# Performance work log

Measured on AMD Instinct MI355X. Metric: run time of the kernel, lower is better.

## Reference

```python
import jax, jax.numpy as jnp
import numpy as np

B, N, F, D, K = 128, 512, 64, 64, 20  # batch, nodes, input_dim, dim, topk


def setup_inputs() -> dict:
    key = jax.random.key(0)
    ks = jax.random.split(key, 9)
    s = 1.0 / np.sqrt(D)
    return dict(
        data=jax.random.normal(ks[0], (B, N, F), jnp.float32),
        org_edge_index=jax.random.randint(ks[1], (2, 1024), 0, N),
        embed=jax.random.normal(ks[2], (N, D), jnp.float32),
        W_lin=jax.random.normal(ks[3], (F, D), jnp.float32) / np.sqrt(F),
        att_i=jax.random.normal(ks[4], (D,), jnp.float32) * s,
        att_j=jax.random.normal(ks[5], (D,), jnp.float32) * s,
        att_em_i=jax.random.normal(ks[6], (D,), jnp.float32) * s,
        att_em_j=jax.random.normal(ks[7], (D,), jnp.float32) * s,
        gnn_bias=jnp.zeros((D,), jnp.float32),
        bn1_gamma=jnp.ones((D,), jnp.float32),
        bn1_beta=jnp.zeros((D,), jnp.float32),
        bn2_gamma=jnp.ones((D,), jnp.float32),
        bn2_beta=jnp.zeros((D,), jnp.float32),
        out_W=jax.random.normal(ks[8], (D, 1), jnp.float32) * s,
        out_b=jnp.zeros((1,), jnp.float32),
    )


def reference(data, embed, W_lin, att_i, att_j, att_em_i, att_em_j, gnn_bias,
              bn1_gamma, bn1_beta, bn2_gamma, bn2_beta, out_W, out_b,
              org_edge_index):
    eps = 1e-5
    slope = 0.2  # LeakyReLU negative slope (PyG GATConv default)
    BN_ = B * N

    # Encoder -> learned graph: cosine similarity + topk (GDN-style)
    e_norm = embed / (jnp.linalg.norm(embed, axis=-1, keepdims=True) + 1e-12)
    weight_arr = e_norm @ e_norm.T                      # [N, N]
    _, topk_idx = jax.lax.top_k(weight_arr, K)          # [N, K]

    src = topk_idx.reshape(-1)                          # gated_j (message source)
    dst = jnp.repeat(jnp.arange(N), K)                  # gated_i (message dest)
    self_mask = src == dst                              # remove_self_loops

    # batched edge index (block-diagonal over batch)
    offs = (jnp.arange(B) * N)[:, None]
    src_b = (src[None, :] + offs).reshape(-1)
    dst_b = (dst[None, :] + offs).reshape(-1)
    mask_b = jnp.tile(self_mask, B)

    # add_self_loops for all B*N nodes
    loops = jnp.arange(BN_)
    src_all = jnp.concatenate([src_b, loops])
    dst_all = jnp.concatenate([dst_b, loops])
    mask_all = jnp.concatenate([mask_b, jnp.zeros((BN_,), bool)])

    # GraphLayer: linear transform + embedding-augmented attention
    x = data.reshape(BN_, F)
    g = x @ W_lin                                       # [BN, D]
    emb_all = jnp.tile(embed, (B, 1))                   # [BN, D]
    s_i = g @ att_i + emb_all @ att_em_i                # per-node dest score
    s_j = g @ att_j + emb_all @ att_em_j                # per-node src score
    logits = jax.nn.leaky_relu(s_i[dst_all] + s_j[src_all], slope)
    logits = jnp.where(mask_all, -jnp.inf, logits)      # removed self edges

    # softmax over incoming edges of each destination node
    m = jax.ops.segment_max(logits, dst_all, num_segments=BN_)
    ex = jnp.exp(logits - m[dst_all])
    denom = jax.ops.segment_sum(ex, dst_all, num_segments=BN_)
    attn = ex / denom[dst_all]

    agg = jax.ops.segment_sum(g[src_all] * attn[:, None], dst_all,
                              num_segments=BN_) + gnn_bias  # [BN, D]

    # BatchNorm1d (batch stats) + ReLU
    mu = agg.mean(0)
    var = agg.var(0)
    h = jax.nn.relu((agg - mu) / jnp.sqrt(var + eps) * bn1_gamma + bn1_beta)

    # multiply by node embedding, channel BN over (batch, node), ReLU
    h = h.reshape(B, N, D) * embed[None]
    mu2 = h.mean(axis=(0, 1))
    var2 = h.var(axis=(0, 1))
    h = jax.nn.relu((h - mu2) / jnp.sqrt(var2 + eps) * bn2_gamma + bn2_beta)

    # OutLayer (layer_num=1): Linear(D, 1)
    out = (h @ out_W + out_b).reshape(B, N)
    return out
```

## Files before the change

kernel.cpp:

```cpp
#include <hip/hip_runtime.h>
#include <math.h>

#define Bsz 128
#define Nn  512
#define Fd  64
#define Dd  64
#define Kk  20
#define BN  (Bsz*Nn)
#define NCPY 32
#define ET_STRIDE 129
#define SMEM_BYTES (64*ET_STRIDE*4 + 256*4)

__device__ __forceinline__ float leaky(float v){ return (v >= 0.f) ? v : 0.2f*v; }

__device__ __forceinline__ int wave_argmax_idx(float v, int idx){
  int vi = __float_as_int(v);
#define DPP_STEP(CTRL) { \
    int nv = __builtin_amdgcn_update_dpp(vi,  vi,  CTRL, 0xF, 0xF, false); \
    int ni = __builtin_amdgcn_update_dpp(idx, idx, CTRL, 0xF, 0xF, false); \
    float fnv = __int_as_float(nv), fov = __int_as_float(vi); \
    bool take = (fnv > fov) || ((fnv == fov) && (ni < idx)); \
    vi = take ? nv : vi; idx = take ? ni : idx; \
  }
  DPP_STEP(0x111)
  DPP_STEP(0x112)
  DPP_STEP(0x114)
  DPP_STEP(0x118)
  DPP_STEP(0x142)
  DPP_STEP(0x143)
#undef DPP_STEP
  return __builtin_amdgcn_readlane(idx, 63);
}

__global__ __launch_bounds__(256) void k1(const float* __restrict__ x,
    const float* __restrict__ W, const float* __restrict__ embed,
    const float* __restrict__ att_i, const float* __restrict__ att_j,
    const float* __restrict__ aem_i, const float* __restrict__ aem_j,
    float* __restrict__ g, float* __restrict__ s_i, float* __restrict__ s_j,
    int* __restrict__ topk){
  __shared__ __align__(16) char smem[SMEM_BYTES];
  int tid = threadIdx.x, b = blockIdx.x;

  if (b >= 128){
    int bl = b - 128;
    float4* sW   = (float4*)smem;
    float4* sai  = (float4*)(smem + 16384);
    float4* saj  = sai + 16;
    float4* semi = saj + 16;
    float4* semj = semi + 16;
    const float4* W4 = (const float4*)W;
    #pragma unroll
    for (int t = 0; t < 4; t++) sW[tid + 256*t] = W4[tid + 256*t];
    if (tid < 16){
      sai[tid]  = ((const float4*)att_i)[tid];
      saj[tid]  = ((const float4*)att_j)[tid];
      semi[tid] = ((const float4*)aem_i)[tid];
      semj[tid] = ((const float4*)aem_j)[tid];
    }
    __syncthreads();
    int rowgrp = tid >> 4, cg = tid & 15;
    int row0 = bl*64 + rowgrp*4;
    float4 acc0={0,0,0,0}, acc1={0,0,0,0}, acc2={0,0,0,0}, acc3={0,0,0,0};
    const float4* xr0 = (const float4*)(x + (row0+0)*Fd);
    const float4* xr1 = (const float4*)(x + (row0+1)*Fd);
    const float4* xr2 = (const float4*)(x + (row0+2)*Fd);
    const float4* xr3 = (const float4*)(x + (row0+3)*Fd);
    for (int qk = 0; qk < 16; qk++){
      float4 x0 = xr0[qk], x1 = xr1[qk], x2 = xr2[qk], x3 = xr3[qk];
      float xs0[4] = {x0.x,x0.y,x0.z,x0.w};
      float xs1[4] = {x1.x,x1.y,x1.z,x1.w};
      float xs2[4] = {x2.x,x2.y,x2.z,x2.w};
      float xs3[4] = {x3.x,x3.y,x3.z,x3.w};
      #pragma unroll
      for (int s = 0; s < 4; s++){
        float4 w4 = sW[(4*qk + s)*16 + cg];
        acc0.x += xs0[s]*w4.x; acc0.y += xs0[s]*w4.y; acc0.z += xs0[s]*w4.z; acc0.w += xs0[s]*w4.w;
        acc1.x += xs1[s]*w4.x; acc1.y += xs1[s]*w4.y; acc1.z += xs1[s]*w4.z; acc1.w += xs1[s]*w4.w;
        acc2.x += xs2[s]*w4.x; acc2.y += xs2[s]*w4.y; acc2.z += xs2[s]*w4.z; acc2.w += xs2[s]*w4.w;
        acc3.x += xs3[s]*w4.x; acc3.y += xs3[s]*w4.y; acc3.z += xs3[s]*w4.z; acc3.w += xs3[s]*w4.w;
      }
    }
    float4 ai = sai[cg], aj = saj[cg], emi = semi[cg], emj = semj[cg];
    float4 avv[4] = {acc0, acc1, acc2, acc3};
    #pragma unroll
    for (int r = 0; r < 4; r++){
      int row = row0 + r;
      int node = row & (Nn-1);
      float4 a4 = avv[r];
      float4 e4 = ((const float4*)embed)[node*16 + cg];
      float si = a4.x*ai.x + a4.y*ai.y + a4.z*ai.z + a4.w*ai.w
               + e4.x*emi.x + e4.y*emi.y + e4.z*emi.z + e4.w*emi.w;
      float sj = a4.x*aj.x + a4.y*aj.y + a4.z*aj.z + a4.w*aj.w
               + e4.x*emj.x + e4.y*emj.y + e4.z*emj.z + e4.w*emj.w;
      #pragma unroll
      for (int o = 1; o < 16; o <<= 1){
        si += __shfl_xor(si, o, 64);
        sj += __shfl_xor(sj, o, 64);
      }
      if (cg == 0){ s_i[row] = si; s_j[row] = sj; }
      ((float4*)(g + row*Dd))[cg] = a4;
    }
  } else {
    int bb = b;
    float* eT = (float*)smem;
    float* se = (float*)(smem + 64*ET_STRIDE*4);
    int wv = tid >> 6, lane = tid & 63;
    se[tid] = embed[bb*256 + tid];
    const float4* emb4 = (const float4*)embed;
    float av[8];
    #pragma unroll
    for (int tt = 0; tt < 4; tt++){
      float4 stg[8];
      #pragma unroll
      for (int j = 0; j < 8; j++)
        stg[j] = emb4[tt*2048 + j*256 + tid];
      __syncthreads();
      #pragma unroll
      for (int j = 0; j < 8; j++){
        float4 v = stg[j];
        float ss = v.x*v.x + v.y*v.y + v.z*v.z + v.w*v.w;
        #pragma unroll
        for (int o = 1; o < 16; o <<= 1) ss += __shfl_xor(ss, o, 64);
        float rn = 1.f/(sqrtf(ss) + 1e-12f);
        int row_local = j*16 + (tid >> 4);
        int d0 = (tid & 15)*4;
        eT[(d0+0)*ET_STRIDE + row_local] = v.x*rn;
        eT[(d0+1)*ET_STRIDE + row_local] = v.y*rn;
        eT[(d0+2)*ET_STRIDE + row_local] = v.z*rn;
        eT[(d0+3)*ET_STRIDE + row_local] = v.w*rn;
      }
      __syncthreads();
      const float4* sef4 = (const float4*)(se + wv*64);
      float a0 = 0.f, a1 = 0.f;
      #pragma unroll
      for (int d4 = 0; d4 < 16; d4++){
        float4 q4 = sef4[d4];
        int d = d4*4;
        a0 += q4.x*eT[(d+0)*ET_STRIDE + lane] + q4.y*eT[(d+1)*ET_STRIDE + lane]
            + q4.z*eT[(d+2)*ET_STRIDE + lane] + q4.w*eT[(d+3)*ET_STRIDE + lane];
        a1 += q4.x*eT[(d+0)*ET_STRIDE + 64 + lane] + q4.y*eT[(d+1)*ET_STRIDE + 64 + lane]
            + q4.z*eT[(d+2)*ET_STRIDE + 64 + lane] + q4.w*eT[(d+3)*ET_STRIDE + 64 + lane];
      }
      av[2*tt]   = a0;
      av[2*tt+1] = a1;
    }
    int row = bb*4 + wv;
    #pragma unroll 1
    for (int t = 0; t < Kk; t++){
      float bv = av[0]; int br = 0;
      #pragma unroll
      for (int rep = 1; rep < 8; rep++)
        if (av[rep] > bv){ bv = av[rep]; br = rep; }
      int ci = br*64 + lane;
      int win = wave_argmax_idx(bv, ci);
      if (lane == 0) topk[row*Kk + t] = win;
      int wr = win >> 6;
      if ((win & 63) == lane){
        #pragma unroll
        for (int rep = 0; rep < 8; rep++)
          if (rep == wr) av[rep] = -INFINITY;
      }
    }
  }
}

__global__ __launch_bounds__(256) void k2(const float* __restrict__ g,
    const float* __restrict__ s_i, const float* __restrict__ s_j,
    const int* __restrict__ topk, const float* __restrict__ bias,
    float* __restrict__ agg, float* __restrict__ stats){
  __shared__ float  swt[4][4][24];
  __shared__ int    sji[4][4][24];
  __shared__ float4 sred_s[4][16], sred_q[4][16];
  __shared__ float4 sbias[16];
  int tid = threadIdx.x, wv = tid >> 6, lane = tid & 63;
  if (tid < 16) sbias[tid] = ((const float4*)bias)[tid];
  __syncthreads();
  int bid = blockIdx.x;
  int xcd = bid & 7, q = bid >> 3;
  int batch = xcd*16 + (q & 15);
  int six = q >> 4;
  int base = batch*Nn;
  int node0 = six*32 + wv*8;
  const float4* g4 = (const float4*)g;
  int h = lane >> 4, c = lane & 15;
  int half = lane >> 5, ln = lane & 31;
  float4 s4 = {0,0,0,0}, q4 = {0,0,0,0};
  #pragma unroll 1
  for (int gI = 0; gI < 2; gI++){
    #pragma unroll
    for (int pr = 0; pr < 2; pr++){
      int node = node0 + gI*4 + pr*2 + half;
      int dest = base + node;
      float si_d = s_i[dest];
      float lg = -INFINITY; int j = node;
      if (ln < Kk){
        j = topk[node*Kk + ln];
        if (j != node) lg = leaky(si_d + s_j[base + j]);
      } else if (ln == Kk){
        lg = leaky(si_d + s_j[dest]);
      }
      float m = lg;
      #pragma unroll
      for (int o = 16; o; o >>= 1) m = fmaxf(m, __shfl_xor(m, o, 64));
      float e_ = (ln <= Kk) ? __expf(lg - m) : 0.f;
      float denom = e_;
      #pragma unroll
      for (int o = 16; o; o >>= 1) denom += __shfl_xor(denom, o, 64);
      if (ln < 24){
        swt[wv][pr*2+half][ln] = (ln <= Kk) ? e_/denom : 0.f;
        sji[wv][pr*2+half][ln] = j;
      }
    }
    float la[24]; int ja[24];
    const float4* lv = (const float4*)swt[wv][h];
    const int4*   jv = (const int4*)sji[wv][h];
    #pragma unroll
    for (int qq = 0; qq < 6; qq++){
      float4 f = lv[qq]; la[4*qq]=f.x; la[4*qq+1]=f.y; la[4*qq+2]=f.z; la[4*qq+3]=f.w;
      int4  ii = jv[qq]; ja[4*qq]=ii.x; ja[4*qq+1]=ii.y; ja[4*qq+2]=ii.z; ja[4*qq+3]=ii.w;
    }
    float4 acc = sbias[c];
    #pragma unroll
    for (int e = 0; e <= Kk; e++){
      float4 gv = g4[(base + ja[e])*16 + c];
      acc.x += la[e]*gv.x; acc.y += la[e]*gv.y; acc.z += la[e]*gv.z; acc.w += la[e]*gv.w;
    }
    int dest = base + node0 + gI*4 + h;
    ((float4*)agg)[dest*16 + c] = acc;
    s4.x += acc.x; s4.y += acc.y; s4.z += acc.z; s4.w += acc.w;
    q4.x += acc.x*acc.x; q4.y += acc.y*acc.y; q4.z += acc.z*acc.z; q4.w += acc.w*acc.w;
  }
  #pragma unroll
  for (int o = 16; o <= 32; o <<= 1){
    s4.x += __shfl_xor(s4.x,o,64); s4.y += __shfl_xor(s4.y,o,64);
    s4.z += __shfl_xor(s4.z,o,64); s4.w += __shfl_xor(s4.w,o,64);
    q4.x += __shfl_xor(q4.x,o,64); q4.y += __shfl_xor(q4.y,o,64);
    q4.z += __shfl_xor(q4.z,o,64); q4.w += __shfl_xor(q4.w,o,64);
  }
  if (lane < 16){ sred_s[wv][lane] = s4; sred_q[wv][lane] = q4; }
  __syncthreads();
  float* sc = stats + (bid & (NCPY-1))*256;
  if (wv == 0 && lane < 16){
    float4 a = sred_s[0][lane];
    #pragma unroll
    for (int w = 1; w < 4; w++){ float4 t = sred_s[w][lane]; a.x+=t.x; a.y+=t.y; a.z+=t.z; a.w+=t.w; }
    atomicAdd(&sc[lane*4+0], a.x); atomicAdd(&sc[lane*4+1], a.y);
    atomicAdd(&sc[lane*4+2], a.z); atomicAdd(&sc[lane*4+3], a.w);
  }
  if (wv == 1 && lane < 16){
    float4 a = sred_q[0][lane];
    #pragma unroll
    for (int w = 1; w < 4; w++){ float4 t = sred_q[w][lane]; a.x+=t.x; a.y+=t.y; a.z+=t.z; a.w+=t.w; }
    atomicAdd(&sc[64+lane*4+0], a.x); atomicAdd(&sc[64+lane*4+1], a.y);
    atomicAdd(&sc[64+lane*4+2], a.z); atomicAdd(&sc[64+lane*4+3], a.w);
  }
}

__global__ __launch_bounds__(256) void k3(const float* __restrict__ agg,
    const float* __restrict__ embed, const float* __restrict__ bn1g,
    const float* __restrict__ bn1b, float* __restrict__ stats){
  __shared__ float ssc[64], ssh[64];
  __shared__ float4 sred_s[4][16], sred_q[4][16];
  int tid = threadIdx.x;
  if (tid < 64){
    float s = 0.f, qq = 0.f;
    #pragma unroll
    for (int x = 0; x < NCPY; x++){ s += stats[x*256 + tid]; qq += stats[x*256 + 64 + tid]; }
    float mu = s*(1.f/BN), var = qq*(1.f/BN) - mu*mu;
    float sc = bn1g[tid]/sqrtf(var + 1e-5f);
    ssc[tid] = sc; ssh[tid] = bn1b[tid] - mu*sc;
  }
  __syncthreads();
  int gt = blockIdx.x*256 + tid;
  int c = gt & 15, r0 = gt >> 4;
  int wv = tid >> 6, lane = tid & 63;
  float4 sc1 = ((const float4*)ssc)[c], sh1 = ((const float4*)ssh)[c];
  float4 e4 = ((const float4*)embed)[(r0 & (Nn-1))*16 + c];
  float4 s4 = {0,0,0,0}, q4 = {0,0,0,0};
  const float4* a4 = (const float4*)agg;
  for (int r = r0; r < BN; r += 32768){
    float4 v = a4[r*16 + c];
    v.x = fmaxf(v.x*sc1.x+sh1.x, 0.f)*e4.x;
    v.y = fmaxf(v.y*sc1.y+sh1.y, 0.f)*e4.y;
    v.z = fmaxf(v.z*sc1.z+sh1.z, 0.f)*e4.z;
    v.w = fmaxf(v.w*sc1.w+sh1.w, 0.f)*e4.w;
    s4.x += v.x; s4.y += v.y; s4.z += v.z; s4.w += v.w;
    q4.x += v.x*v.x; q4.y += v.y*v.y; q4.z += v.z*v.z; q4.w += v.w*v.w;
  }
  #pragma unroll
  for (int o = 16; o <= 32; o <<= 1){
    s4.x += __shfl_xor(s4.x,o,64); s4.y += __shfl_xor(s4.y,o,64);
    s4.z += __shfl_xor(s4.z,o,64); s4.w += __shfl_xor(s4.w,o,64);
    q4.x += __shfl_xor(q4.x,o,64); q4.y += __shfl_xor(q4.y,o,64);
    q4.z += __shfl_xor(q4.z,o,64); q4.w += __shfl_xor(q4.w,o,64);
  }
  if (lane < 16){ sred_s[wv][lane] = s4; sred_q[wv][lane] = q4; }
  __syncthreads();
  float* sc = stats + (blockIdx.x & (NCPY-1))*256;
  if (wv == 0 && lane < 16){
    float4 a = sred_s[0][lane];
    #pragma unroll
    for (int w = 1; w < 4; w++){ float4 t = sred_s[w][lane]; a.x+=t.x; a.y+=t.y; a.z+=t.z; a.w+=t.w; }
    atomicAdd(&sc[128+lane*4+0], a.x); atomicAdd(&sc[128+lane*4+1], a.y);
    atomicAdd(&sc[128+lane*4+2], a.z); atomicAdd(&sc[128+lane*4+3], a.w);
  }
  if (wv == 1 && lane < 16){
    float4 a = sred_q[0][lane];
    #pragma unroll
    for (int w = 1; w < 4; w++){ float4 t = sred_q[w][lane]; a.x+=t.x; a.y+=t.y; a.z+=t.z; a.w+=t.w; }
    atomicAdd(&sc[192+lane*4+0], a.x); atomicAdd(&sc[192+lane*4+1], a.y);
    atomicAdd(&sc[192+lane*4+2], a.z); atomicAdd(&sc[192+lane*4+3], a.w);
  }
}

__global__ __launch_bounds__(256) void k4(const float* __restrict__ agg,
    const float* __restrict__ embed, const float* __restrict__ bn1g,
    const float* __restrict__ bn1b, const float* __restrict__ bn2g,
    const float* __restrict__ bn2b, const float* __restrict__ outW,
    const float* __restrict__ outb, const float* __restrict__ stats,
    float* __restrict__ out){
  __shared__ float ssc1[64], ssh1[64], ssc2[64], ssh2[64];
  int tid = threadIdx.x;
  if (tid < 64){
    float s1=0.f, q1=0.f, s2=0.f, q2=0.f;
    #pragma unroll
    for (int x = 0; x < NCPY; x++){
      const float* p = stats + x*256;
      s1 += p[tid]; q1 += p[64+tid]; s2 += p[128+tid]; q2 += p[192+tid];
    }
    float mu1 = s1*(1.f/BN), var1 = q1*(1.f/BN) - mu1*mu1;
    float sc1 = bn1g[tid]/sqrtf(var1 + 1e-5f);
    ssc1[tid] = sc1; ssh1[tid] = bn1b[tid] - mu1*sc1;
    float mu2 = s2*(1.f/BN), var2 = q2*(1.f/BN) - mu2*mu2;
    float sc2 = bn2g[tid]/sqrtf(var2 + 1e-5f);
    ssc2[tid] = sc2; ssh2[tid] = bn2b[tid] - mu2*sc2;
  }
  __syncthreads();
  int gt = blockIdx.x*256 + tid;
  int c = gt & 15, r0 = gt >> 4;
  float4 sc1 = ((const float4*)ssc1)[c], sh1 = ((const float4*)ssh1)[c];
  float4 sc2 = ((const float4*)ssc2)[c], sh2 = ((const float4*)ssh2)[c];
  float4 ow  = ((const float4*)outW)[c];
  float ob = outb[0];
  float4 e4 = ((const float4*)embed)[(r0 & (Nn-1))*16 + c];
  const float4* a4 = (const float4*)agg;
  for (int r = r0; r < BN; r += 32768){
    float4 v = a4[r*16 + c];
    v.x = fmaxf(v.x*sc1.x+sh1.x, 0.f)*e4.x;
    v.y = fmaxf(v.y*sc1.y+sh1.y, 0.f)*e4.y;
    v.z = fmaxf(v.z*sc1.z+sh1.z, 0.f)*e4.z;
    v.w = fmaxf(v.w*sc1.w+sh1.w, 0.f)*e4.w;
    float t = fmaxf(v.x*sc2.x+sh2.x, 0.f)*ow.x
            + fmaxf(v.y*sc2.y+sh2.y, 0.f)*ow.y
            + fmaxf(v.z*sc2.z+sh2.z, 0.f)*ow.z
            + fmaxf(v.w*sc2.w+sh2.w, 0.f)*ow.w;
    #pragma unroll
    for (int o = 1; o < 16; o <<= 1) t += __shfl_xor(t, o, 64);
    if (c == 0) out[r] = t + ob;
  }
}

extern "C" void kernel_launch(void* const* d_in, const int* in_sizes, int n_in,
                              void* d_out, int out_size, void* d_ws, size_t ws_size,
                              hipStream_t stream){
  const float* data  = (const float*)d_in[0];
  const float* embed = (const float*)d_in[2];
  const float* W_lin = (const float*)d_in[3];
  const float* att_i = (const float*)d_in[4];
  const float* att_j = (const float*)d_in[5];
  const float* aem_i = (const float*)d_in[6];
  const float* aem_j = (const float*)d_in[7];
  const float* bias  = (const float*)d_in[8];
  const float* g1    = (const float*)d_in[9];
  const float* b1    = (const float*)d_in[10];
  const float* g2    = (const float*)d_in[11];
  const float* b2    = (const float*)d_in[12];
  const float* outW  = (const float*)d_in[13];
  const float* outb  = (const float*)d_in[14];
  float* out = (float*)d_out;

  float* ws    = (float*)d_ws;
  float* g     = ws;
  float* agg   = ws + 4194304;
  float* s_i   = ws + 8388608;
  float* s_j   = s_i + 65536;
  int*   topk  = (int*)(s_j + 65536);
  float* stats = (float*)(topk + Nn*Kk);

  hipMemsetAsync(stats, 0, NCPY*256*sizeof(float), stream);
  k1<<<1152, 256, 0, stream>>>(data, W_lin, embed, att_i, att_j, aem_i, aem_j,
                               g, s_i, s_j, topk);
  k2<<<2048, 256, 0, stream>>>(g, s_i, s_j, topk, bias, agg, stats);
  k3<<<2048, 256, 0, stream>>>(agg, embed, g1, b1, stats);
  k4<<<2048, 256, 0, stream>>>(agg, embed, g1, b1, g2, b2, outW, outb, stats, out);
}
```

Before: 151.8 us.

## Fuse aggregation and both BatchNorm passes into one persistent kernel with grid barriers

Merges k2, k3 and k4 into a single kernel of 1024 blocks. Each block keeps its aggregated rows in registers, so the agg buffer is never written or read back. The BatchNorm statistics are finalized through atomic arrival counters and spin-wait grid barriers. The separate memset is replaced by zeroing the stats and control words inside k1. This removes two kernel launches and two full passes over the 16 MB agg tensor, at the cost of requiring all 1024 blocks to be co-resident; otherwise the spin-wait can deadlock.

```diff
diff --git a/kernel.cpp b/kernel.cpp
--- a/kernel.cpp
+++ b/kernel.cpp
@@ -8,6 +8,7 @@
 #define Kk  20
 #define BN  (Bsz*Nn)
 #define NCPY 32
+#define NBLK 1024u
 #define ET_STRIDE 129
 #define SMEM_BYTES (64*ET_STRIDE*4 + 256*4)
 
@@ -37,7 +38,7 @@
     const float* __restrict__ att_i, const float* __restrict__ att_j,
     const float* __restrict__ aem_i, const float* __restrict__ aem_j,
     float* __restrict__ g, float* __restrict__ s_i, float* __restrict__ s_j,
-    int* __restrict__ topk){
+    int* __restrict__ topk, float* __restrict__ stats){
   __shared__ __align__(16) char smem[SMEM_BYTES];
   int tid = threadIdx.x, b = blockIdx.x;
 
@@ -58,7 +59,7 @@
       semj[tid] = ((const float4*)aem_j)[tid];
     }
     __syncthreads();
-    int rowgrp = tid >> 4, cg = tid & 15;
+    int rowgrp = tid >> 4, cg_ = tid & 15;
     int row0 = bl*64 + rowgrp*4;
     float4 acc0={0,0,0,0}, acc1={0,0,0,0}, acc2={0,0,0,0}, acc3={0,0,0,0};
     const float4* xr0 = (const float4*)(x + (row0+0)*Fd);
@@ -73,21 +74,21 @@
       float xs3[4] = {x3.x,x3.y,x3.z,x3.w};
       #pragma unroll
       for (int s = 0; s < 4; s++){
-        float4 w4 = sW[(4*qk + s)*16 + cg];
+        float4 w4 = sW[(4*qk + s)*16 + cg_];
         acc0.x += xs0[s]*w4.x; acc0.y += xs0[s]*w4.y; acc0.z += xs0[s]*w4.z; acc0.w += xs0[s]*w4.w;
         acc1.x += xs1[s]*w4.x; acc1.y += xs1[s]*w4.y; acc1.z += xs1[s]*w4.z; acc1.w += xs1[s]*w4.w;
         acc2.x += xs2[s]*w4.x; acc2.y += xs2[s]*w4.y; acc2.z += xs2[s]*w4.z; acc2.w += xs2[s]*w4.w;
         acc3.x += xs3[s]*w4.x; acc3.y += xs3[s]*w4.y; acc3.z += xs3[s]*w4.z; acc3.w += xs3[s]*w4.w;
       }
     }
-    float4 ai = sai[cg], aj = saj[cg], emi = semi[cg], emj = semj[cg];
+    float4 ai = sai[cg_], aj = saj[cg_], emi = semi[cg_], emj = semj[cg_];
     float4 avv[4] = {acc0, acc1, acc2, acc3};
     #pragma unroll
     for (int r = 0; r < 4; r++){
       int row = row0 + r;
       int node = row & (Nn-1);
       float4 a4 = avv[r];
-      float4 e4 = ((const float4*)embed)[node*16 + cg];
+      float4 e4 = ((const float4*)embed)[node*16 + cg_];
       float si = a4.x*ai.x + a4.y*ai.y + a4.z*ai.z + a4.w*ai.w
                + e4.x*emi.x + e4.y*emi.y + e4.z*emi.z + e4.w*emi.w;
       float sj = a4.x*aj.x + a4.y*aj.y + a4.z*aj.z + a4.w*aj.w
@@ -97,11 +98,15 @@
         si += __shfl_xor(si, o, 64);
         sj += __shfl_xor(sj, o, 64);
       }
-      if (cg == 0){ s_i[row] = si; s_j[row] = sj; }
-      ((float4*)(g + row*Dd))[cg] = a4;
+      if (cg_ == 0){ s_i[row] = si; s_j[row] = sj; }
+      ((float4*)(g + row*Dd))[cg_] = a4;
     }
   } else {
     int bb = b;
+    if (b == 0){
+      #pragma unroll 1
+      for (int i = tid; i < NCPY*256 + 16; i += 256) stats[i] = 0.f;
+    }
     float* eT = (float*)smem;
     float* se = (float*)(smem + 64*ET_STRIDE*4);
     int wv = tid >> 6, lane = tid & 63;
@@ -164,29 +169,37 @@
   }
 }
 
-__global__ __launch_bounds__(256) void k2(const float* __restrict__ g,
+__global__ __launch_bounds__(256, 4) void k234(const float* __restrict__ g,
     const float* __restrict__ s_i, const float* __restrict__ s_j,
     const int* __restrict__ topk, const float* __restrict__ bias,
-    float* __restrict__ agg, float* __restrict__ stats){
+    const float* __restrict__ embed, const float* __restrict__ bn1g,
+    const float* __restrict__ bn1b, const float* __restrict__ bn2g,
+    const float* __restrict__ bn2b, const float* __restrict__ outW,
+    const float* __restrict__ outb, float* __restrict__ stats,
+    unsigned* __restrict__ ctrl, float* __restrict__ bnp,
+    float* __restrict__ out){
   __shared__ float  swt[4][4][24];
   __shared__ int    sji[4][4][24];
   __shared__ float4 sred_s[4][16], sred_q[4][16];
   __shared__ float4 sbias[16];
+  __shared__ float  ssc[64], ssh[64];
+  __shared__ int    slast;
   int tid = threadIdx.x, wv = tid >> 6, lane = tid & 63;
   if (tid < 16) sbias[tid] = ((const float4*)bias)[tid];
   __syncthreads();
   int bid = blockIdx.x;
   int xcd = bid & 7, q = bid >> 3;
   int batch = xcd*16 + (q & 15);
-  int six = q >> 4;
+  int eighth = q >> 4;
   int base = batch*Nn;
-  int node0 = six*32 + wv*8;
+  int node0 = eighth*64 + wv*16;
   const float4* g4 = (const float4*)g;
   int h = lane >> 4, c = lane & 15;
   int half = lane >> 5, ln = lane & 31;
+  float4 accs[4];
   float4 s4 = {0,0,0,0}, q4 = {0,0,0,0};
-  #pragma unroll 1
-  for (int gI = 0; gI < 2; gI++){
+  #pragma unroll
+  for (int gI = 0; gI < 4; gI++){
     #pragma unroll
     for (int pr = 0; pr < 2; pr++){
       int node = node0 + gI*4 + pr*2 + half;
@@ -225,8 +238,7 @@
       float4 gv = g4[(base + ja[e])*16 + c];
       acc.x += la[e]*gv.x; acc.y += la[e]*gv.y; acc.z += la[e]*gv.z; acc.w += la[e]*gv.w;
     }
-    int dest = base + node0 + gI*4 + h;
-    ((float4*)agg)[dest*16 + c] = acc;
+    accs[gI] = acc;
     s4.x += acc.x; s4.y += acc.y; s4.z += acc.z; s4.w += acc.w;
     q4.x += acc.x*acc.x; q4.y += acc.y*acc.y; q4.z += acc.z*acc.z; q4.w += acc.w*acc.w;
   }
@@ -254,49 +266,62 @@
     atomicAdd(&sc[64+lane*4+0], a.x); atomicAdd(&sc[64+lane*4+1], a.y);
     atomicAdd(&sc[64+lane*4+2], a.z); atomicAdd(&sc[64+lane*4+3], a.w);
   }
-}
-
-__global__ __launch_bounds__(256) void k3(const float* __restrict__ agg,
-    const float* __restrict__ embed, const float* __restrict__ bn1g,
-    const float* __restrict__ bn1b, float* __restrict__ stats){
-  __shared__ float ssc[64], ssh[64];
-  __shared__ float4 sred_s[4][16], sred_q[4][16];
-  int tid = threadIdx.x;
+  __syncthreads();
+  if (tid == 0){
+    unsigned prev = __hip_atomic_fetch_add(&ctrl[0], 1u, __ATOMIC_ACQ_REL, __HIP_MEMORY_SCOPE_AGENT);
+    slast = (prev == NBLK - 1u);
+  }
+  __syncthreads();
+  if (slast){
+    if (tid < 64){
+      float s = 0.f, qq = 0.f;
+      #pragma unroll
+      for (int x = 0; x < NCPY; x++){
+        s  += __hip_atomic_load(&stats[x*256 + tid],      __ATOMIC_RELAXED, __HIP_MEMORY_SCOPE_AGENT);
+        qq += __hip_atomic_load(&stats[x*256 + 64 + tid], __ATOMIC_RELAXED, __HIP_MEMORY_SCOPE_AGENT);
+      }
+      float mu = s*(1.f/BN), var = qq*(1.f/BN) - mu*mu;
+      float scv = bn1g[tid]/sqrtf(var + 1e-5f);
+      __hip_atomic_store(&bnp[tid],      scv,                __ATOMIC_RELAXED, __HIP_MEMORY_SCOPE_AGENT);
+      __hip_atomic_store(&bnp[64 + tid], bn1b[tid] - mu*scv, __ATOMIC_RELAXED, __HIP_MEMORY_SCOPE_AGENT);
+    }
+    __syncthreads();
+    if (tid == 0) __hip_atomic_store(&ctrl[1], 1u, __ATOMIC_RELEASE, __HIP_MEMORY_SCOPE_AGENT);
+  }
+  if (tid == 0){
+    while (__hip_atomic_load(&ctrl[1], __ATOMIC_ACQUIRE, __HIP_MEMORY_SCOPE_AGENT) == 0u)
+      __builtin_amdgcn_s_sleep(8);
+  }
+  __syncthreads();
   if (tid < 64){
-    float s = 0.f, qq = 0.f;
-    #pragma unroll
-    for (int x = 0; x < NCPY; x++){ s += stats[x*256 + tid]; qq += stats[x*256 + 64 + tid]; }
-    float mu = s*(1.f/BN), var = qq*(1.f/BN) - mu*mu;
-    float sc = bn1g[tid]/sqrtf(var + 1e-5f);
-    ssc[tid] = sc; ssh[tid] = bn1b[tid] - mu*sc;
-  }
-  __syncthreads();
-  int gt = blockIdx.x*256 + tid;
-  int c = gt & 15, r0 = gt >> 4;
-  int wv = tid >> 6, lane = tid & 63;
+    ssc[tid] = __hip_atomic_load(&bnp[tid],      __ATOMIC_RELAXED, __HIP_MEMORY_SCOPE_AGENT);
+    ssh[tid] = __hip_atomic_load(&bnp[64 + tid], __ATOMIC_RELAXED, __HIP_MEMORY_SCOPE_AGENT);
+  }
+  __syncthreads();
   float4 sc1 = ((const float4*)ssc)[c], sh1 = ((const float4*)ssh)[c];
-  float4 e4 = ((const float4*)embed)[(r0 & (Nn-1))*16 + c];
-  float4 s4 = {0,0,0,0}, q4 = {0,0,0,0};
-  const float4* a4 = (const float4*)agg;
-  for (int r = r0; r < BN; r += 32768){
-    float4 v = a4[r*16 + c];
+  float4 s4b = {0,0,0,0}, q4b = {0,0,0,0};
+  #pragma unroll
+  for (int gI = 0; gI < 4; gI++){
+    int node = node0 + gI*4 + h;
+    float4 e4 = ((const float4*)embed)[node*16 + c];
+    float4 v = accs[gI];
     v.x = fmaxf(v.x*sc1.x+sh1.x, 0.f)*e4.x;
     v.y = fmaxf(v.y*sc1.y+sh1.y, 0.f)*e4.y;
     v.z = fmaxf(v.z*sc1.z+sh1.z, 0.f)*e4.z;
     v.w = fmaxf(v.w*sc1.w+sh1.w, 0.f)*e4.w;
-    s4.x += v.x; s4.y += v.y; s4.z += v.z; s4.w += v.w;
-    q4.x += v.x*v.x; q4.y += v.y*v.y; q4.z += v.z*v.z; q4.w += v.w*v.w;
+    accs[gI] = v;
+    s4b.x += v.x; s4b.y += v.y; s4b.z += v.z; s4b.w += v.w;
+    q4b.x += v.x*v.x; q4b.y += v.y*v.y; q4b.z += v.z*v.z; q4b.w += v.w*v.w;
   }
   #pragma unroll
   for (int o = 16; o <= 32; o <<= 1){
-    s4.x += __shfl_xor(s4.x,o,64); s4.y += __shfl_xor(s4.y,o,64);
-    s4.z += __shfl_xor(s4.z,o,64); s4.w += __shfl_xor(s4.w,o,64);
-    q4.x += __shfl_xor(q4.x,o,64); q4.y += __shfl_xor(q4.y,o,64);
-    q4.z += __shfl_xor(q4.z,o,64); q4.w += __shfl_xor(q4.w,o,64);
-  }
-  if (lane < 16){ sred_s[wv][lane] = s4; sred_q[wv][lane] = q4; }
-  __syncthreads();
-  float* sc = stats + (blockIdx.x & (NCPY-1))*256;
+    s4b.x += __shfl_xor(s4b.x,o,64); s4b.y += __shfl_xor(s4b.y,o,64);
+    s4b.z += __shfl_xor(s4b.z,o,64); s4b.w += __shfl_xor(s4b.w,o,64);
+    q4b.x += __shfl_xor(q4b.x,o,64); q4b.y += __shfl_xor(q4b.y,o,64);
+    q4b.z += __shfl_xor(q4b.z,o,64); q4b.w += __shfl_xor(q4b.w,o,64);
+  }
+  if (lane < 16){ sred_s[wv][lane] = s4b; sred_q[wv][lane] = q4b; }
+  __syncthreads();
   if (wv == 0 && lane < 16){
     float4 a = sred_s[0][lane];
     #pragma unroll
@@ -311,52 +336,51 @@
     atomicAdd(&sc[192+lane*4+0], a.x); atomicAdd(&sc[192+lane*4+1], a.y);
     atomicAdd(&sc[192+lane*4+2], a.z); atomicAdd(&sc[192+lane*4+3], a.w);
   }
-}
-
-__global__ __launch_bounds__(256) void k4(const float* __restrict__ agg,
-    const float* __restrict__ embed, const float* __restrict__ bn1g,
-    const float* __restrict__ bn1b, const float* __restrict__ bn2g,
-    const float* __restrict__ bn2b, const float* __restrict__ outW,
-    const float* __restrict__ outb, const float* __restrict__ stats,
-    float* __restrict__ out){
-  __shared__ float ssc1[64], ssh1[64], ssc2[64], ssh2[64];
-  int tid = threadIdx.x;
+  __syncthreads();
+  if (tid == 0){
+    unsigned prev = __hip_atomic_fetch_add(&ctrl[2], 1u, __ATOMIC_ACQ_REL, __HIP_MEMORY_SCOPE_AGENT);
+    slast = (prev == NBLK - 1u);
+  }
+  __syncthreads();
+  if (slast){
+    if (tid < 64){
+      float s = 0.f, qq = 0.f;
+      #pragma unroll
+      for (int x = 0; x < NCPY; x++){
+        s  += __hip_atomic_load(&stats[x*256 + 128 + tid], __ATOMIC_RELAXED, __HIP_MEMORY_SCOPE_AGENT);
+        qq += __hip_atomic_load(&stats[x*256 + 192 + tid], __ATOMIC_RELAXED, __HIP_MEMORY_SCOPE_AGENT);
+      }
+      float mu = s*(1.f/BN), var = qq*(1.f/BN) - mu*mu;
+      float scv = bn2g[tid]/sqrtf(var + 1e-5f);
+      __hip_atomic_store(&bnp[128 + tid], scv,                __ATOMIC_RELAXED, __HIP_MEMORY_SCOPE_AGENT);
+      __hip_atomic_store(&bnp[192 + tid], bn2b[tid] - mu*scv, __ATOMIC_RELAXED, __HIP_MEMORY_SCOPE_AGENT);
+    }
+    __syncthreads();
+    if (tid == 0) __hip_atomic_store(&ctrl[3], 1u, __ATOMIC_RELEASE, __HIP_MEMORY_SCOPE_AGENT);
+  }
+  if (tid == 0){
+    while (__hip_atomic_load(&ctrl[3], __ATOMIC_ACQUIRE, __HIP_MEMORY_SCOPE_AGENT) == 0u)
+      __builtin_amdgcn_s_sleep(8);
+  }
+  __syncthreads();
   if (tid < 64){
-    float s1=0.f, q1=0.f, s2=0.f, q2=0.f;
-    #pragma unroll
-    for (int x = 0; x < NCPY; x++){
-      const float* p = stats + x*256;
-      s1 += p[tid]; q1 += p[64+tid]; s2 += p[128+tid]; q2 += p[192+tid];
-    }
-    float mu1 = s1*(1.f/BN), var1 = q1*(1.f/BN) - mu1*mu1;
-    float sc1 = bn1g[tid]/sqrtf(var1 + 1e-5f);
-    ssc1[tid] = sc1; ssh1[tid] = bn1b[tid] - mu1*sc1;
-    float mu2 = s2*(1.f/BN), var2 = q2*(1.f/BN) - mu2*mu2;
-    float sc2 = bn2g[tid]/sqrtf(var2 + 1e-5f);
-    ssc2[tid] = sc2; ssh2[tid] = bn2b[tid] - mu2*sc2;
-  }
-  __syncthreads();
-  int gt = blockIdx.x*256 + tid;
-  int c = gt & 15, r0 = gt >> 4;
-  float4 sc1 = ((const float4*)ssc1)[c], sh1 = ((const float4*)ssh1)[c];
-  float4 sc2 = ((const float4*)ssc2)[c], sh2 = ((const float4*)ssh2)[c];
+    ssc[tid] = __hip_atomic_load(&bnp[128 + tid], __ATOMIC_RELAXED, __HIP_MEMORY_SCOPE_AGENT);
+    ssh[tid] = __hip_atomic_load(&bnp[192 + tid], __ATOMIC_RELAXED, __HIP_MEMORY_SCOPE_AGENT);
+  }
+  __syncthreads();
+  float4 sc2 = ((const float4*)ssc)[c], sh2 = ((const float4*)ssh)[c];
   float4 ow  = ((const float4*)outW)[c];
   float ob = outb[0];
-  float4 e4 = ((const float4*)embed)[(r0 & (Nn-1))*16 + c];
-  const float4* a4 = (const float4*)agg;
-  for (int r = r0; r < BN; r += 32768){
-    float4 v = a4[r*16 + c];
-    v.x = fmaxf(v.x*sc1.x+sh1.x, 0.f)*e4.x;
-    v.y = fmaxf(v.y*sc1.y+sh1.y, 0.f)*e4.y;
-    v.z = fmaxf(v.z*sc1.z+sh1.z, 0.f)*e4.z;
-    v.w = fmaxf(v.w*sc1.w+sh1.w, 0.f)*e4.w;
+  #pragma unroll
+  for (int gI = 0; gI < 4; gI++){
+    float4 v = accs[gI];
     float t = fmaxf(v.x*sc2.x+sh2.x, 0.f)*ow.x
             + fmaxf(v.y*sc2.y+sh2.y, 0.f)*ow.y
             + fmaxf(v.z*sc2.z+sh2.z, 0.f)*ow.z
             + fmaxf(v.w*sc2.w+sh2.w, 0.f)*ow.w;
     #pragma unroll
     for (int o = 1; o < 16; o <<= 1) t += __shfl_xor(t, o, 64);
-    if (c == 0) out[r] = t + ob;
+    if (c == 0) out[base + node0 + gI*4 + h] = t + ob;
   }
 }
 
@@ -381,16 +405,15 @@
 
   float* ws    = (float*)d_ws;
   float* g     = ws;
-  float* agg   = ws + 4194304;
   float* s_i   = ws + 8388608;
   float* s_j   = s_i + 65536;
-  int*   topk  = (int*)(s_j + 65536);
-  float* stats = (float*)(topk + Nn*Kk);
-
-  hipMemsetAsync(stats, 0, NCPY*256*sizeof(float), stream);
+  int*   tk    = (int*)(s_j + 65536);
+  float* stats = (float*)(tk + Nn*Kk);
+  unsigned* ctrl = (unsigned*)(stats + NCPY*256);
+  float* bnp   = (float*)(ctrl + 16);
+
   k1<<<1152, 256, 0, stream>>>(data, W_lin, embed, att_i, att_j, aem_i, aem_j,
-                               g, s_i, s_j, topk);
-  k2<<<2048, 256, 0, stream>>>(g, s_i, s_j, topk, bias, agg, stats);
-  k3<<<2048, 256, 0, stream>>>(agg, embed, g1, b1, stats);
-  k4<<<2048, 256, 0, stream>>>(agg, embed, g1, b1, g2, b2, outW, outb, stats, out);
+                               g, s_i, s_j, tk, stats);
+  k234<<<1024, 256, 0, stream>>>(g, s_i, s_j, tk, bias, embed, g1, b1, g2, b2,
+                                 outW, outb, stats, ctrl, bnp, out);
 }
```

After: 596.5 us. 3.93x slower.
